# Optimization experiments

Hardware: AMD Instinct MI355X
Metric: run time of the kernel (lower is better)

Reference implementation:

```python
import jax, jax.numpy as jnp
import numpy as np

N = 50000          # nodes
E = 1_600_000      # edges (avg degree 32)
F_IN = 256
F_OUT = 256
ALPHA = 0.2        # LeakyReLU negative slope


def setup_inputs() -> dict:
    key = jax.random.key(0)
    ks = jax.random.split(key, 7)
    x = jax.random.normal(ks[0], (N, F_IN), dtype=jnp.float32)
    row = jax.random.randint(ks[1], (E,), 0, N, dtype=jnp.int32)  # dst i
    col = jax.random.randint(ks[2], (E,), 0, N, dtype=jnp.int32)  # src j
    W_w = jax.random.normal(ks[3], (F_IN, F_OUT), dtype=jnp.float32) / np.sqrt(F_IN).astype(np.float32)
    W_b = jax.random.normal(ks[4], (F_OUT,), dtype=jnp.float32) * 0.01
    a_w = jax.random.normal(ks[5], (2 * F_OUT,), dtype=jnp.float32) / np.sqrt(2 * F_OUT).astype(np.float32)
    a_b = jax.random.normal(ks[6], (1,), dtype=jnp.float32) * 0.01
    return {"x": x, "W_w": W_w, "W_b": W_b, "a_w": a_w, "a_b": a_b,
            "row": row, "col": col}


def reference(x, W_w, W_b, a_w, a_b, row, col):
    # Wh = W(x): [N, F_OUT]
    Wh = x @ W_w + W_b
    # e[i,j] = leakyrelu(a1 . Wh[j] + a2 . Wh[i] + b)
    # (repeat puts Wh[j] in the first half of the concat, repeat_interleave Wh[i] in the second)
    f_dst_part = Wh @ a_w[:F_OUT]   # contribution of column node j
    f_row_part = Wh @ a_w[F_OUT:]   # contribution of row node i
    e = f_dst_part[col] + f_row_part[row] + a_b[0]          # [E]
    e = jnp.where(e > 0, e, ALPHA * e)                      # LeakyReLU
    # sparse softmax over dim=1 (segment = row i), adjacency values are 1.0
    m = jax.ops.segment_max(e, row, num_segments=N)         # [N]
    ex = jnp.exp(e - m[row])
    denom = jax.ops.segment_sum(ex, row, num_segments=N)    # [N]
    att = ex / denom[row]                                   # [E]
    # h'[i] = sum_j att[i,j] * Wh[j]  (spmm), empty rows stay zero
    h_prime = jax.ops.segment_sum(att[:, None] * Wh[col], row, num_segments=N)
    return jax.nn.relu(h_prime)
```

## Files before the change

### kernel.cpp

```cpp
#include <hip/hip_runtime.h>
#include <math.h>

#define N_NODES 50000
#define N_EDGES 1600000
#define F 256
#define ALPHA 0.2f
#define NP 50048
#define NB 196
#define CAP 10240
#define EPB 4096
#define NAB ((N_EDGES + EPB - 1) / EPB)
#define GEMM_BLOCKS 782
#define FVEC_SLOTS 2048
#define PULL_BLOCKS 2048
#define NW_TOT (PULL_BLOCKS * 4)
#define NPW 7
#define NBIN 8

typedef short bf16x8 __attribute__((ext_vector_type(8)));
typedef float f32x4 __attribute__((ext_vector_type(4)));
typedef _Float16 half4 __attribute__((ext_vector_type(4)));
typedef _Float16 half8 __attribute__((ext_vector_type(8)));

__device__ __forceinline__ unsigned short f2bf(float f) {
  union { float f; unsigned u; } v; v.f = f;
  unsigned u = v.u;
  return (unsigned short)((u + 0x7fffu + ((u >> 16) & 1u)) >> 16);
}

__device__ __forceinline__ unsigned short f2h_bits(float f) {
  union { _Float16 h; unsigned short u; } v;
  v.h = (_Float16)f;
  return v.u;
}

__device__ __forceinline__ float h_bits2f(unsigned short u) {
  union { _Float16 h; unsigned short u; } v;
  v.u = u;
  return (float)v.h;
}

__global__ __launch_bounds__(256) void prep_w(const float* __restrict__ W,
                                              const float* __restrict__ a_w,
                                              const float* __restrict__ W_b,
                                              const float* __restrict__ a_b,
                                              unsigned short* __restrict__ Wt,
                                              float* __restrict__ wa,
                                              float* __restrict__ cb,
                                              int* __restrict__ gcur) {
  if (blockIdx.x == 64) {
    if (threadIdx.x < NB) gcur[threadIdx.x] = 0;
    return;
  }
  const int lane = threadIdx.x & 63, w = threadIdx.x >> 6;
  const int k = blockIdx.x * 4 + w;
  float4 wv = *(const float4*)(W + (size_t)k * F + lane * 4);
  float4 a1 = *(const float4*)(a_w + lane * 4);
  float4 a2 = *(const float4*)(a_w + F + lane * 4);
  Wt[(size_t)(lane * 4 + 0) * F + k] = f2bf(wv.x);
  Wt[(size_t)(lane * 4 + 1) * F + k] = f2bf(wv.y);
  Wt[(size_t)(lane * 4 + 2) * F + k] = f2bf(wv.z);
  Wt[(size_t)(lane * 4 + 3) * F + k] = f2bf(wv.w);
  float s1 = wv.x * a1.x + wv.y * a1.y + wv.z * a1.z + wv.w * a1.w;
  float s2 = wv.x * a2.x + wv.y * a2.y + wv.z * a2.z + wv.w * a2.w;
#pragma unroll
  for (int off = 32; off > 0; off >>= 1) {
    s1 += __shfl_down(s1, off, 64);
    s2 += __shfl_down(s2, off, 64);
  }
  if (lane == 0) { wa[k] = s1; wa[F + k] = s2; }
  if (blockIdx.x == 0 && w == 0) {
    float4 b = *(const float4*)(W_b + lane * 4);
    float t1 = b.x * (a1.x + a2.x) + b.y * (a1.y + a2.y) +
               b.z * (a1.z + a2.z) + b.w * (a1.w + a2.w);
#pragma unroll
    for (int off = 32; off > 0; off >>= 1) t1 += __shfl_down(t1, off, 64);
    if (lane == 0) cb[0] = t1 + a_b[0];
  }
}

#define LDSK 72
__global__ __launch_bounds__(256) void gemm_fvec_binA2(
    const float* __restrict__ x,
    const unsigned short* __restrict__ Wt,
    const float* __restrict__ bias,
    const float* __restrict__ wa,
    const int* __restrict__ row,
    const int* __restrict__ col,
    _Float16* __restrict__ Wh,
    float* __restrict__ f_dst,
    float* __restrict__ f_row,
    int* __restrict__ gcur,
    unsigned* __restrict__ gstage) {
  __shared__ char smem[2 * 128 * LDSK * 2];
  if (blockIdx.x < GEMM_BLOCKS) {
    short* As = (short*)smem;
    short* Bs = As + 128 * LDSK;
    const int tid = threadIdx.x;
    const int lane = tid & 63;
    const int w = tid >> 6;
    const int wm = w >> 1, wn = w & 1;
    const int m0 = (blockIdx.x >> 1) * 128;
    const int n0 = (blockIdx.x & 1) * 128;
    f32x4 acc[4][4] = {{{0.f, 0.f, 0.f, 0.f}}};
    const int srow = tid >> 3;
    const int schunk = tid & 7;
    for (int k0 = 0; k0 < F; k0 += 64) {
#pragma unroll
      for (int i = 0; i < 4; ++i) {
        int r = i * 32 + srow;
        int gm = m0 + r; if (gm > N_NODES - 1) gm = N_NODES - 1;
        const float* src = x + (size_t)gm * F + k0 + schunk * 8;
        float4 lo = *(const float4*)src;
        float4 hi = *(const float4*)(src + 4);
        bf16x8 v;
        v[0] = (short)f2bf(lo.x); v[1] = (short)f2bf(lo.y);
        v[2] = (short)f2bf(lo.z); v[3] = (short)f2bf(lo.w);
        v[4] = (short)f2bf(hi.x); v[5] = (short)f2bf(hi.y);
        v[6] = (short)f2bf(hi.z); v[7] = (short)f2bf(hi.w);
        *(bf16x8*)&As[r * LDSK + schunk * 8] = v;
        *(bf16x8*)&Bs[r * LDSK + schunk * 8] =
            *(const bf16x8*)(Wt + (size_t)(n0 + r) * F + k0 + schunk * 8);
      }
      __syncthreads();
#pragma unroll
      for (int kk = 0; kk < 64; kk += 32) {
        const int rowsel = lane & 15;
        const int ksel = kk + (lane >> 4) * 8;
        bf16x8 af[4], bfr[4];
#pragma unroll
        for (int t = 0; t < 4; ++t) {
          af[t] = *(bf16x8*)&As[(wm * 64 + t * 16 + rowsel) * LDSK + ksel];
          bfr[t] = *(bf16x8*)&Bs[(wn * 64 + t * 16 + rowsel) * LDSK + ksel];
        }
#pragma unroll
        for (int mi = 0; mi < 4; ++mi)
#pragma unroll
          for (int nj = 0; nj < 4; ++nj)
            acc[mi][nj] = __builtin_amdgcn_mfma_f32_16x16x32_bf16(
                af[mi], bfr[nj], acc[mi][nj], 0, 0, 0);
      }
      __syncthreads();
    }
    const int crow = (lane >> 4) * 4;
    const int ccol = lane & 15;
#pragma unroll
    for (int nj = 0; nj < 4; ++nj) {
      int gc = n0 + wn * 64 + nj * 16 + ccol;
      float bv = bias[gc];
#pragma unroll
      for (int mi = 0; mi < 4; ++mi) {
        int gr = m0 + wm * 64 + mi * 16 + crow;
#pragma unroll
        for (int r = 0; r < 4; ++r)
          Wh[(size_t)(gr + r) * F + gc] = (_Float16)(acc[mi][nj][r] + bv);
      }
    }
    return;
  }
  if (blockIdx.x < GEMM_BLOCKS + NAB) {
    int* h = (int*)smem;
    int* lofs = h + NB;
    int* lcur = lofs + NB;
    int* gb = lcur + NB;
    unsigned* stage = (unsigned*)(gb + NB);
    const int t = threadIdx.x;
    for (int i = t; i < NB; i += 256) { h[i] = 0; lcur[i] = 0; }
    __syncthreads();
    const int base = (blockIdx.x - GEMM_BLOCKS) * EPB;
    const int cnt = min(EPB, N_EDGES - base);
#pragma unroll
    for (int j = 0; j < 16; ++j) {
      int k = base + j * 256 + t;
      if (k < N_EDGES) atomicAdd(&h[row[k] >> 8], 1);
    }
    __syncthreads();
    if (t == 0) {
      int run = 0;
      for (int i = 0; i < NB; ++i) { lofs[i] = run; run += h[i]; }
    }
    __syncthreads();
    if (t < NB && h[t] > 0) gb[t] = atomicAdd(&gcur[t], h[t]);
    __syncthreads();
#pragma unroll
    for (int j = 0; j < 16; ++j) {
      int k = base + j * 256 + t;
      if (k < N_EDGES) {
        int r = row[k], b = r >> 8;
        int lp = lofs[b] + atomicAdd(&lcur[b], 1);
        stage[lp] = ((unsigned)b << 24) | ((unsigned)(r & 255) << 16) |
                    (unsigned)col[k];
      }
    }
    __syncthreads();
#pragma unroll
    for (int j = 0; j < 16; ++j) {
      int s = j * 256 + t;
      if (s < cnt) {
        unsigned wv = stage[s];
        int b = wv >> 24;
        gstage[(size_t)b * CAP + gb[b] + (s - lofs[b])] = wv & 0x00FFFFFFu;
      }
    }
    return;
  }
  const int lane = threadIdx.x & 63, w = threadIdx.x >> 6;
  const int slot = blockIdx.x - GEMM_BLOCKS - NAB;
  float4 v1 = *(const float4*)(wa + lane * 4);
  float4 v2 = *(const float4*)(wa + F + lane * 4);
  for (int node = slot * 4 + w; node < N_NODES; node += FVEC_SLOTS * 4) {
    float4 xv = *(const float4*)(x + (size_t)node * F + lane * 4);
    float s1 = xv.x * v1.x + xv.y * v1.y + xv.z * v1.z + xv.w * v1.w;
    float s2 = xv.x * v2.x + xv.y * v2.y + xv.z * v2.z + xv.w * v2.w;
#pragma unroll
    for (int off = 32; off > 0; off >>= 1) {
      s1 += __shfl_down(s1, off, 64);
      s2 += __shfl_down(s2, off, 64);
    }
    if (lane == 0) { f_dst[node] = s1; f_row[node] = s2; }
  }
}

__global__ __launch_bounds__(512) void binB(const int* __restrict__ gcur,
                                            const unsigned* __restrict__ gstage,
                                            const float* __restrict__ f_dst,
                                            const float* __restrict__ f_row,
                                            const float* __restrict__ cb,
                                            int2* __restrict__ rsc,
                                            float* __restrict__ inv_denom,
                                            unsigned* __restrict__ csr,
                                            int* __restrict__ bstart) {
  __shared__ int cnt2[2048];
  __shared__ int cur2[2048];
  __shared__ int rcnt[256], rbase[256];
  __shared__ float dsum[256];
  const int t = threadIdx.x;
  const int b = blockIdx.x;
  for (int i = t; i < 2048; i += 512) cnt2[i] = 0;
  if (t < 256) dsum[t] = 0.f;
  __syncthreads();
  const int nb = gcur[b];
  const int start = b * CAP;
  const float cbs = cb[0];
  for (int s = t; s < nb; s += 512) {
    unsigned wv = gstage[start + s];
    int key = (((wv >> 16) & 255) << 3) | ((wv & 0xFFFFu) >> 13);
    atomicAdd(&cnt2[key], 1);
  }
  __syncthreads();
  if (t < 256) {
    int tot = 0;
#pragma unroll
    for (int q = 0; q < 8; ++q) tot += cnt2[t * 8 + q];
    rcnt[t] = tot;
  }
  __syncthreads();
  if (t == 0) {
    int run = 0;
    for (int i = 0; i < 256; ++i) { rbase[i] = run; run += rcnt[i]; }
  }
  __syncthreads();
  if (t < 256) {
    int base = start + rbase[t];
    int g = (b << 8) + t;
    if (g < N_NODES) rsc[g] = make_int2(base, rcnt[t]);
    int run = base;
    int bs[8];
#pragma unroll
    for (int q = 0; q < 8; ++q) {
      cur2[t * 8 + q] = run;
      bs[q] = run;
      run += cnt2[t * 8 + q];
    }
    if (g < N_NODES) {
      *(int4*)&bstart[(size_t)g * 8]     = make_int4(bs[0], bs[1], bs[2], bs[3]);
      *(int4*)&bstart[(size_t)g * 8 + 4] = make_int4(bs[4], bs[5], bs[6], bs[7]);
    }
  }
  __syncthreads();
  for (int s = t; s < nb; s += 512) {
    unsigned wv = gstage[start + s];
    int lr = (wv >> 16) & 255;
    int c = wv & 0xFFFF;
    float ev = f_dst[c] + f_row[(b << 8) + lr] + cbs;
    ev = ev > 0.f ? ev : ALPHA * ev;
    float ex = __expf(ev);
    int p = atomicAdd(&cur2[(lr << 3) | (c >> 13)], 1);
    csr[p] = ((unsigned)f2h_bits(ex) << 16) | (unsigned)c;
    atomicAdd(&dsum[lr], ex);
  }
  __syncthreads();
  if (t < 256) {
    int g = (b << 8) + t;
    if (g < N_NODES) inv_denom[g] = (rcnt[t] > 0) ? (1.0f / dsum[t]) : 0.f;
  }
}

__global__ __launch_bounds__(256) void gat_pull(const int2* __restrict__ rsc,
                                                const unsigned* __restrict__ csr,
                                                const float* __restrict__ inv_denom,
                                                const int* __restrict__ bstart,
                                                const _Float16* __restrict__ Wh,
                                                float* __restrict__ out) {
  __shared__ int sb[4 * NPW * 9];
  const int lane = threadIdx.x & 63;
  const int wv_id = threadIdx.x >> 6;
  const int wid = blockIdx.x * 4 + wv_id;
  for (int e = threadIdx.x; e < 4 * NPW * 9; e += 256) {
    int w = e / (NPW * 9);
    int rem = e - w * (NPW * 9);
    int jn = rem / 9, q = rem - jn * 9;
    int i = blockIdx.x * 4 + w + jn * NW_TOT;
    int v = 0;
    if (i < N_NODES) {
      if (q < 8) v = bstart[(size_t)i * 8 + q];
      else { int2 rc = rsc[i]; v = rc.x + rc.y; }
    }
    sb[e] = v;
  }
  __syncthreads();
  const int* mb = &sb[wv_id * NPW * 9];
  const char* whb = (const char*)Wh;
  const unsigned chanoff = (unsigned)lane * 8u;
  const int l16 = lane & 15;
  float a0[NPW], a1[NPW], a2[NPW], a3[NPW];
#pragma unroll
  for (int jn = 0; jn < NPW; ++jn) a0[jn] = a1[jn] = a2[jn] = a3[jn] = 0.f;
  for (int q = 0; q < NBIN; ++q) {
    int pp = mb[q], pe = mb[q + 1];
    unsigned cw0 = 0;
    if (pp + l16 < pe) cw0 = csr[pp + l16];
#pragma unroll
    for (int jn = 0; jn < NPW; ++jn) {
      const int cpp = pp, cpe = pe;
      unsigned cw = cw0;
      if (jn + 1 < NPW) {
        pp = mb[(jn + 1) * 9 + q];
        pe = mb[(jn + 1) * 9 + q + 1];
        cw0 = 0;
        if (pp + l16 < pe) cw0 = csr[pp + l16];
      }
      const int len = cpe - cpp;
      for (int done = 0; done < len; done += 16) {
        if (done) {
          cw = 0;
          if (cpp + done + l16 < cpe) cw = csr[cpp + done + l16];
        }
        int cl = len - done;
        if (cl > 16) cl = 16;
        for (int jb = 0; jb < cl; jb += 4) {
          const int j1 = (jb + 1 < cl) ? jb + 1 : 0;
          const int j2 = (jb + 2 < cl) ? jb + 2 : 0;
          const int j3 = (jb + 3 < cl) ? jb + 3 : 0;
          unsigned w0 = __builtin_amdgcn_readlane(cw, jb);
          unsigned w1 = __builtin_amdgcn_readlane(cw, j1);
          unsigned w2 = __builtin_amdgcn_readlane(cw, j2);
          unsigned w3 = __builtin_amdgcn_readlane(cw, j3);
          half4 v0 = *(const half4*)(whb + (size_t)(w0 & 0xFFFFu) * 512u + chanoff);
          half4 v1 = *(const half4*)(whb + (size_t)(w1 & 0xFFFFu) * 512u + chanoff);
          half4 v2 = *(const half4*)(whb + (size_t)(w2 & 0xFFFFu) * 512u + chanoff);
          half4 v3 = *(const half4*)(whb + (size_t)(w3 & 0xFFFFu) * 512u + chanoff);
          float x0 = h_bits2f((unsigned short)(w0 >> 16));
          float x1 = (jb + 1 < cl) ? h_bits2f((unsigned short)(w1 >> 16)) : 0.f;
          float x2 = (jb + 2 < cl) ? h_bits2f((unsigned short)(w2 >> 16)) : 0.f;
          float x3 = (jb + 3 < cl) ? h_bits2f((unsigned short)(w3 >> 16)) : 0.f;
          a0[jn] += x0 * (float)v0[0]; a1[jn] += x0 * (float)v0[1];
          a2[jn] += x0 * (float)v0[2]; a3[jn] += x0 * (float)v0[3];
          a0[jn] += x1 * (float)v1[0]; a1[jn] += x1 * (float)v1[1];
          a2[jn] += x1 * (float)v1[2]; a3[jn] += x1 * (float)v1[3];
          a0[jn] += x2 * (float)v2[0]; a1[jn] += x2 * (float)v2[1];
          a2[jn] += x2 * (float)v2[2]; a3[jn] += x2 * (float)v2[3];
          a0[jn] += x3 * (float)v3[0]; a1[jn] += x3 * (float)v3[1];
          a2[jn] += x3 * (float)v3[2]; a3[jn] += x3 * (float)v3[3];
        }
      }
    }
  }
#pragma unroll
  for (int jn = 0; jn < NPW; ++jn) {
    int i = wid + jn * NW_TOT;
    if (i >= N_NODES) continue;
    const float inv = inv_denom[i];
    float4 o = make_float4(fmaxf(a0[jn] * inv, 0.f), fmaxf(a1[jn] * inv, 0.f),
                           fmaxf(a2[jn] * inv, 0.f), fmaxf(a3[jn] * inv, 0.f));
    ((float4*)out)[(size_t)i * 64 + lane] = o;
  }
}

extern "C" void kernel_launch(void* const* d_in, const int* in_sizes, int n_in,
                              void* d_out, int out_size, void* d_ws, size_t ws_size,
                              hipStream_t stream) {
  const float* x   = (const float*)d_in[0];
  const float* W_w = (const float*)d_in[1];
  const float* W_b = (const float*)d_in[2];
  const float* a_w = (const float*)d_in[3];
  const float* a_b = (const float*)d_in[4];
  const int*   row = (const int*)d_in[5];
  const int*   col = (const int*)d_in[6];
  float* out = (float*)d_out;

  float* ws = (float*)d_ws;
  size_t off = 0;
  _Float16* Wh = (_Float16*)(ws + off); off += (size_t)NP * F / 2;
  unsigned short* Wt = (unsigned short*)(ws + off); off += (F * F) / 2;
  float* wa = ws + off;            off += 2 * F;
  float* cb = ws + off;            off += 8;
  float* f_dst = ws + off;         off += NP;
  float* f_row = ws + off;         off += NP;
  int* gcur = (int*)(ws + off);    off += NB;
  int2* rsc = (int2*)(ws + off);   off += 2 * (size_t)NP;
  float* inv_denom = (float*)(ws + off); off += NP;
  unsigned* gstage = (unsigned*)(ws + off); off += (size_t)NB * CAP;
  unsigned* csr = (unsigned*)(ws + off); off += (size_t)NB * CAP;
  int* bstart = (int*)(ws + off);  off += (size_t)NP * 8;
  (void)ws_size; (void)in_sizes; (void)n_in; (void)out_size;

  hipLaunchKernelGGL(prep_w, dim3(65), dim3(256), 0, stream, W_w, a_w, W_b,
                     a_b, Wt, wa, cb, gcur);
  hipLaunchKernelGGL(gemm_fvec_binA2, dim3(GEMM_BLOCKS + NAB + FVEC_SLOTS),
                     dim3(256), 0, stream, x, Wt, W_b, wa, row, col, Wh,
                     f_dst, f_row, gcur, gstage);
  hipLaunchKernelGGL(binB, dim3(NB), dim3(512), 0, stream, gcur, gstage,
                     f_dst, f_row, cb, rsc, inv_denom, csr, bstart);
  hipLaunchKernelGGL(gat_pull, dim3(PULL_BLOCKS), dim3(256), 0, stream,
                     rsc, csr, inv_denom, bstart, Wh, out);
}
```

Baseline: 265.3 us.

## Fuse attention score dot products into GEMM epilogue and halve row-bin size

Removes the separate f_dst/f_row pass, which re-read x with the folded W·a vectors. Instead the GEMM epilogue computes dot products of each Wh tile with a_w, reduces them across lanes and atomically adds partial sums into zeroed f_dst/f_row buffers. The bias term now enters through Wh, so cb holds only a_b. Row bins also shrink from 256 to 128 rows, doubling the bin count so binB runs 392 blocks, each with a smaller per-block workload. In exchange it adds global float atomics from two column-half blocks per row and makes the summation order nondeterministic.

```diff
diff --git a/kernel.cpp b/kernel.cpp
--- a/kernel.cpp
+++ b/kernel.cpp
@@ -6,12 +6,11 @@
 #define F 256
 #define ALPHA 0.2f
 #define NP 50048
-#define NB 196
-#define CAP 10240
+#define NB 392
+#define CAP 5632
 #define EPB 4096
 #define NAB ((N_EDGES + EPB - 1) / EPB)
 #define GEMM_BLOCKS 782
-#define FVEC_SLOTS 2048
 #define PULL_BLOCKS 2048
 #define NW_TOT (PULL_BLOCKS * 4)
 #define NPW 7
@@ -45,38 +44,31 @@
                                               const float* __restrict__ W_b,
                                               const float* __restrict__ a_b,
                                               unsigned short* __restrict__ Wt,
-                                              float* __restrict__ wa,
+                                              float* __restrict__ f_dst,
+                                              float* __restrict__ f_row,
                                               float* __restrict__ cb,
                                               int* __restrict__ gcur) {
   if (blockIdx.x == 64) {
-    if (threadIdx.x < NB) gcur[threadIdx.x] = 0;
+    for (int i = threadIdx.x; i < NB; i += 256) gcur[i] = 0;
+    return;
+  }
+  if (blockIdx.x > 64) {
+    int idx = (blockIdx.x - 65) * 256 + threadIdx.x;
+    if (idx < NP / 4) {
+      ((float4*)f_dst)[idx] = make_float4(0.f, 0.f, 0.f, 0.f);
+      ((float4*)f_row)[idx] = make_float4(0.f, 0.f, 0.f, 0.f);
+    }
     return;
   }
   const int lane = threadIdx.x & 63, w = threadIdx.x >> 6;
   const int k = blockIdx.x * 4 + w;
   float4 wv = *(const float4*)(W + (size_t)k * F + lane * 4);
-  float4 a1 = *(const float4*)(a_w + lane * 4);
-  float4 a2 = *(const float4*)(a_w + F + lane * 4);
   Wt[(size_t)(lane * 4 + 0) * F + k] = f2bf(wv.x);
   Wt[(size_t)(lane * 4 + 1) * F + k] = f2bf(wv.y);
   Wt[(size_t)(lane * 4 + 2) * F + k] = f2bf(wv.z);
   Wt[(size_t)(lane * 4 + 3) * F + k] = f2bf(wv.w);
-  float s1 = wv.x * a1.x + wv.y * a1.y + wv.z * a1.z + wv.w * a1.w;
-  float s2 = wv.x * a2.x + wv.y * a2.y + wv.z * a2.z + wv.w * a2.w;
-#pragma unroll
-  for (int off = 32; off > 0; off >>= 1) {
-    s1 += __shfl_down(s1, off, 64);
-    s2 += __shfl_down(s2, off, 64);
-  }
-  if (lane == 0) { wa[k] = s1; wa[F + k] = s2; }
-  if (blockIdx.x == 0 && w == 0) {
-    float4 b = *(const float4*)(W_b + lane * 4);
-    float t1 = b.x * (a1.x + a2.x) + b.y * (a1.y + a2.y) +
-               b.z * (a1.z + a2.z) + b.w * (a1.w + a2.w);
-#pragma unroll
-    for (int off = 32; off > 0; off >>= 1) t1 += __shfl_down(t1, off, 64);
-    if (lane == 0) cb[0] = t1 + a_b[0];
-  }
+  if (blockIdx.x == 0 && threadIdx.x == 0) cb[0] = a_b[0];
+  (void)W_b;
 }
 
 #define LDSK 72
@@ -84,7 +76,7 @@
     const float* __restrict__ x,
     const unsigned short* __restrict__ Wt,
     const float* __restrict__ bias,
-    const float* __restrict__ wa,
+    const float* __restrict__ aw,
     const int* __restrict__ row,
     const int* __restrict__ col,
     _Float16* __restrict__ Wh,
@@ -144,21 +136,48 @@
     }
     const int crow = (lane >> 4) * 4;
     const int ccol = lane & 15;
+    float s1[16], s2[16];
+#pragma unroll
+    for (int t = 0; t < 16; ++t) { s1[t] = 0.f; s2[t] = 0.f; }
 #pragma unroll
     for (int nj = 0; nj < 4; ++nj) {
       int gc = n0 + wn * 64 + nj * 16 + ccol;
       float bv = bias[gc];
+      float a1v = aw[gc];
+      float a2v = aw[F + gc];
 #pragma unroll
       for (int mi = 0; mi < 4; ++mi) {
         int gr = m0 + wm * 64 + mi * 16 + crow;
 #pragma unroll
-        for (int r = 0; r < 4; ++r)
-          Wh[(size_t)(gr + r) * F + gc] = (_Float16)(acc[mi][nj][r] + bv);
-      }
+        for (int r = 0; r < 4; ++r) {
+          float wh = acc[mi][nj][r] + bv;
+          Wh[(size_t)(gr + r) * F + gc] = (_Float16)wh;
+          s1[mi * 4 + r] += wh * a1v;
+          s2[mi * 4 + r] += wh * a2v;
+        }
+      }
+    }
+#pragma unroll
+    for (int t = 0; t < 16; ++t) {
+#pragma unroll
+      for (int off = 8; off > 0; off >>= 1) {
+        s1[t] += __shfl_xor(s1[t], off, 64);
+        s2[t] += __shfl_xor(s2[t], off, 64);
+      }
+    }
+    if (ccol == 0) {
+#pragma unroll
+      for (int mi = 0; mi < 4; ++mi)
+#pragma unroll
+        for (int r = 0; r < 4; ++r) {
+          int gr = m0 + wm * 64 + mi * 16 + crow + r;
+          atomicAdd(&f_dst[gr], s1[mi * 4 + r]);
+          atomicAdd(&f_row[gr], s2[mi * 4 + r]);
+        }
     }
     return;
   }
-  if (blockIdx.x < GEMM_BLOCKS + NAB) {
+  {
     int* h = (int*)smem;
     int* lofs = h + NB;
     int* lcur = lofs + NB;
@@ -172,7 +191,7 @@
 #pragma unroll
     for (int j = 0; j < 16; ++j) {
       int k = base + j * 256 + t;
-      if (k < N_EDGES) atomicAdd(&h[row[k] >> 8], 1);
+      if (k < N_EDGES) atomicAdd(&h[row[k] >> 7], 1);
     }
     __syncthreads();
     if (t == 0) {
@@ -180,15 +199,16 @@
       for (int i = 0; i < NB; ++i) { lofs[i] = run; run += h[i]; }
     }
     __syncthreads();
-    if (t < NB && h[t] > 0) gb[t] = atomicAdd(&gcur[t], h[t]);
+    for (int i = t; i < NB; i += 256)
+      if (h[i] > 0) gb[i] = atomicAdd(&gcur[i], h[i]);
     __syncthreads();
 #pragma unroll
     for (int j = 0; j < 16; ++j) {
       int k = base + j * 256 + t;
       if (k < N_EDGES) {
-        int r = row[k], b = r >> 8;
+        int r = row[k], b = r >> 7;
         int lp = lofs[b] + atomicAdd(&lcur[b], 1);
-        stage[lp] = ((unsigned)b << 24) | ((unsigned)(r & 255) << 16) |
+        stage[lp] = ((unsigned)b << 23) | ((unsigned)(r & 127) << 16) |
                     (unsigned)col[k];
       }
     }
@@ -198,26 +218,10 @@
       int s = j * 256 + t;
       if (s < cnt) {
         unsigned wv = stage[s];
-        int b = wv >> 24;
-        gstage[(size_t)b * CAP + gb[b] + (s - lofs[b])] = wv & 0x00FFFFFFu;
-      }
-    }
-    return;
-  }
-  const int lane = threadIdx.x & 63, w = threadIdx.x >> 6;
-  const int slot = blockIdx.x - GEMM_BLOCKS - NAB;
-  float4 v1 = *(const float4*)(wa + lane * 4);
-  float4 v2 = *(const float4*)(wa + F + lane * 4);
-  for (int node = slot * 4 + w; node < N_NODES; node += FVEC_SLOTS * 4) {
-    float4 xv = *(const float4*)(x + (size_t)node * F + lane * 4);
-    float s1 = xv.x * v1.x + xv.y * v1.y + xv.z * v1.z + xv.w * v1.w;
-    float s2 = xv.x * v2.x + xv.y * v2.y + xv.z * v2.z + xv.w * v2.w;
-#pragma unroll
-    for (int off = 32; off > 0; off >>= 1) {
-      s1 += __shfl_down(s1, off, 64);
-      s2 += __shfl_down(s2, off, 64);
-    }
-    if (lane == 0) { f_dst[node] = s1; f_row[node] = s2; }
+        int b = wv >> 23;
+        gstage[(size_t)b * CAP + gb[b] + (s - lofs[b])] = wv & 0x007FFFFFu;
+      }
+    }
   }
 }
 
@@ -230,25 +234,25 @@
                                             float* __restrict__ inv_denom,
                                             unsigned* __restrict__ csr,
                                             int* __restrict__ bstart) {
-  __shared__ int cnt2[2048];
-  __shared__ int cur2[2048];
-  __shared__ int rcnt[256], rbase[256];
-  __shared__ float dsum[256];
+  __shared__ int cnt2[1024];
+  __shared__ int cur2[1024];
+  __shared__ int rcnt[128], rbase[128];
+  __shared__ float dsum[128];
   const int t = threadIdx.x;
   const int b = blockIdx.x;
-  for (int i = t; i < 2048; i += 512) cnt2[i] = 0;
-  if (t < 256) dsum[t] = 0.f;
+  for (int i = t; i < 1024; i += 512) cnt2[i] = 0;
+  if (t < 128) dsum[t] = 0.f;
   __syncthreads();
   const int nb = gcur[b];
   const int start = b * CAP;
   const float cbs = cb[0];
   for (int s = t; s < nb; s += 512) {
     unsigned wv = gstage[start + s];
-    int key = (((wv >> 16) & 255) << 3) | ((wv & 0xFFFFu) >> 13);
+    int key = (((wv >> 16) & 127) << 3) | ((wv & 0xFFFFu) >> 13);
     atomicAdd(&cnt2[key], 1);
   }
   __syncthreads();
-  if (t < 256) {
+  if (t < 128) {
     int tot = 0;
 #pragma unroll
     for (int q = 0; q < 8; ++q) tot += cnt2[t * 8 + q];
@@ -257,12 +261,12 @@
   __syncthreads();
   if (t == 0) {
     int run = 0;
-    for (int i = 0; i < 256; ++i) { rbase[i] = run; run += rcnt[i]; }
-  }
-  __syncthreads();
-  if (t < 256) {
+    for (int i = 0; i < 128; ++i) { rbase[i] = run; run += rcnt[i]; }
+  }
+  __syncthreads();
+  if (t < 128) {
     int base = start + rbase[t];
-    int g = (b << 8) + t;
+    int g = (b << 7) + t;
     if (g < N_NODES) rsc[g] = make_int2(base, rcnt[t]);
     int run = base;
     int bs[8];
@@ -280,9 +284,9 @@
   __syncthreads();
   for (int s = t; s < nb; s += 512) {
     unsigned wv = gstage[start + s];
-    int lr = (wv >> 16) & 255;
+    int lr = (wv >> 16) & 127;
     int c = wv & 0xFFFF;
-    float ev = f_dst[c] + f_row[(b << 8) + lr] + cbs;
+    float ev = f_dst[c] + f_row[(b << 7) + lr] + cbs;
     ev = ev > 0.f ? ev : ALPHA * ev;
     float ex = __expf(ev);
     int p = atomicAdd(&cur2[(lr << 3) | (c >> 13)], 1);
@@ -290,8 +294,8 @@
     atomicAdd(&dsum[lr], ex);
   }
   __syncthreads();
-  if (t < 256) {
-    int g = (b << 8) + t;
+  if (t < 128) {
+    int g = (b << 7) + t;
     if (g < N_NODES) inv_denom[g] = (rcnt[t] > 0) ? (1.0f / dsum[t]) : 0.f;
   }
 }
@@ -403,7 +407,6 @@
   size_t off = 0;
   _Float16* Wh = (_Float16*)(ws + off); off += (size_t)NP * F / 2;
   unsigned short* Wt = (unsigned short*)(ws + off); off += (F * F) / 2;
-  float* wa = ws + off;            off += 2 * F;
   float* cb = ws + off;            off += 8;
   float* f_dst = ws + off;         off += NP;
   float* f_row = ws + off;         off += NP;
@@ -415,10 +418,10 @@
   int* bstart = (int*)(ws + off);  off += (size_t)NP * 8;
   (void)ws_size; (void)in_sizes; (void)n_in; (void)out_size;
 
-  hipLaunchKernelGGL(prep_w, dim3(65), dim3(256), 0, stream, W_w, a_w, W_b,
-                     a_b, Wt, wa, cb, gcur);
-  hipLaunchKernelGGL(gemm_fvec_binA2, dim3(GEMM_BLOCKS + NAB + FVEC_SLOTS),
-                     dim3(256), 0, stream, x, Wt, W_b, wa, row, col, Wh,
+  hipLaunchKernelGGL(prep_w, dim3(114), dim3(256), 0, stream, W_w, a_w, W_b,
+                     a_b, Wt, f_dst, f_row, cb, gcur);
+  hipLaunchKernelGGL(gemm_fvec_binA2, dim3(GEMM_BLOCKS + NAB),
+                     dim3(256), 0, stream, x, Wt, W_b, a_w, row, col, Wh,
                      f_dst, f_row, gcur, gstage);
   hipLaunchKernelGGL(binB, dim3(NB), dim3(512), 0, stream, gcur, gstage,
                      f_dst, f_row, cb, rsc, inv_denom, csr, bstart);
```

After: 271.4 us. 1.02x slower.
